# Performance work log

Measured on AMD Instinct MI355X. Metric: run time of the kernel, lower is better.

Reference implementation:

```python
import jax, jax.numpy as jnp
import numpy as np

NUM_EXPERTS = 8
TOP_K = 2
HIDDEN = 1024
INTER = 3584
B, S = 1, 2048


def setup_inputs() -> dict:
    key = jax.random.key(0)
    k0, k1, k2, k3, k4 = jax.random.split(key, 5)
    scale = 0.02
    return {
        "hidden_states": jax.random.normal(k0, (B, S, HIDDEN), dtype=jnp.float32),
        "gate_w": jax.random.normal(k1, (NUM_EXPERTS, HIDDEN), dtype=jnp.float32) * scale,
        "w1": jax.random.normal(k2, (NUM_EXPERTS, INTER, HIDDEN), dtype=jnp.float32) * scale,
        "w2": jax.random.normal(k3, (NUM_EXPERTS, HIDDEN, INTER), dtype=jnp.float32) * scale,
        "w3": jax.random.normal(k4, (NUM_EXPERTS, INTER, HIDDEN), dtype=jnp.float32) * scale,
    }


def reference(hidden_states, gate_w, w1, w2, w3):
    b, s, h = hidden_states.shape
    x = hidden_states.reshape(-1, h)  # [T, H]
    T = x.shape[0]

    # Router: softmax in float32, take top-k, renormalize (normalize_routing_weights=1)
    router_logits = x @ gate_w.T  # [T, E]
    routing_probs = jax.nn.softmax(router_logits.astype(jnp.float32), axis=-1)
    top_w, top_i = jax.lax.top_k(routing_probs, TOP_K)  # [T, K]
    top_w = top_w / jnp.sum(top_w, axis=-1, keepdims=True)
    top_w = top_w.astype(x.dtype)

    # Dense per-token gate matrix [T, E]: weight if expert selected, else 0.
    rows = jnp.arange(T)[:, None]
    gates = jnp.zeros((T, NUM_EXPERTS), dtype=x.dtype).at[rows, top_i].set(top_w)

    # Equivalent to gather-MLP-scatter: y = sum_e gate[:,e] * SwiGLU_e(x)
    out = jnp.zeros((T, h), dtype=x.dtype)
    for e in range(NUM_EXPERTS):
        hid = jax.nn.silu(x @ w1[e].T) * (x @ w3[e].T)  # [T, F]
        out = out + (hid @ w2[e].T) * gates[:, e:e + 1]
    return out.reshape(b, s, h)
```

## Files before the change

kernel.cpp:

```cpp
#include <hip/hip_runtime.h>
#include <hip/hip_bf16.h>
#include <stdint.h>

#define T_TOKENS 2048
#define HID_DIM 1024
#define INTER 3584
#define NEXP 8
#define PTILES 40

typedef float f32x4 __attribute__((ext_vector_type(4)));
typedef short short8 __attribute__((ext_vector_type(8)));
typedef unsigned short ushort8 __attribute__((ext_vector_type(8)));

#define AS1 __attribute__((address_space(1)))
#define AS3 __attribute__((address_space(3)))

__device__ __forceinline__ void gload_lds16(const void* g, void* l) {
    __builtin_amdgcn_global_load_lds((AS1 void*)g, (AS3 void*)l, 16, 0, 0);
}

__device__ __forceinline__ f32x4 mfma16(short8 a, short8 b, f32x4 c) {
    return __builtin_amdgcn_mfma_f32_16x16x32_bf16(a, b, c, 0, 0, 0);
}

__device__ __forceinline__ unsigned short f2bf(float f) {
    union { __hip_bfloat16 h; unsigned short u; } cv;
    cv.h = __float2bfloat16(f);
    return cv.u;
}

__device__ __forceinline__ ushort8 cvt8(float4 v0, float4 v1) {
    ushort8 u;
    u[0] = f2bf(v0.x); u[1] = f2bf(v0.y); u[2] = f2bf(v0.z); u[3] = f2bf(v0.w);
    u[4] = f2bf(v1.x); u[5] = f2bf(v1.y); u[6] = f2bf(v1.z); u[7] = f2bf(v1.w);
    return u;
}

__global__ __launch_bounds__(256) void pack_w_k(const float* __restrict__ w1, const float* __restrict__ w2,
                                                const float* __restrict__ w3,
                                                unsigned short* __restrict__ w1p,
                                                unsigned short* __restrict__ w3p,
                                                unsigned short* __restrict__ w2p) {
    int which = blockIdx.z;
    int e = blockIdx.y;
    const float* src;
    unsigned short* dst;
    int NT, KT, K;
    if (which == 0) { src = w1; dst = w1p; NT = 56; KT = 16; K = HID_DIM; }
    else if (which == 1) { src = w3; dst = w3p; NT = 56; KT = 16; K = HID_DIM; }
    else { src = w2; dst = w2p; NT = 16; KT = 56; K = INTER; }
    int nt = blockIdx.x % NT;
    int kt = blockIdx.x / NT;

    int col = threadIdx.x & 63;
    int kq = threadIdx.x >> 6;
    const float* s = src + ((size_t)(e * (NT * 64) + nt * 64 + col)) * K + kt * 64 + kq * 16;
    float4 v0 = *reinterpret_cast<const float4*>(s);
    float4 v1 = *reinterpret_cast<const float4*>(s + 4);
    float4 v2 = *reinterpret_cast<const float4*>(s + 8);
    float4 v3 = *reinterpret_cast<const float4*>(s + 12);
    unsigned short* d = dst + ((size_t)(e * NT + nt) * KT + kt) * 4096;
    *reinterpret_cast<ushort8*>(d + ((kq * 2 + 0) * 64 + col) * 8) = cvt8(v0, v1);
    *reinterpret_cast<ushort8*>(d + ((kq * 2 + 1) * 64 + col) * 8) = cvt8(v2, v3);
}

__global__ void router_k(const float* __restrict__ x, const float* __restrict__ gw,
                         int* __restrict__ topk_e, float* __restrict__ topk_w,
                         int* __restrict__ ctl) {
    int lane = threadIdx.x & 63;
    int wid = threadIdx.x >> 6;
    int t = blockIdx.x * 4 + wid;
    const float* xr = x + (size_t)t * HID_DIM;

    float acc[NEXP];
#pragma unroll
    for (int e = 0; e < NEXP; ++e) acc[e] = 0.f;

#pragma unroll
    for (int j = 0; j < 4; ++j) {
        int c = j * 256 + lane * 4;
        float4 v = *reinterpret_cast<const float4*>(xr + c);
#pragma unroll
        for (int e = 0; e < NEXP; ++e) {
            float4 g = *reinterpret_cast<const float4*>(gw + e * HID_DIM + c);
            acc[e] += v.x * g.x + v.y * g.y + v.z * g.z + v.w * g.w;
        }
    }
#pragma unroll
    for (int off = 32; off > 0; off >>= 1)
#pragma unroll
        for (int e = 0; e < NEXP; ++e) acc[e] += __shfl_xor(acc[e], off, 64);

    if (lane == 0) {
        int e0 = 0;
#pragma unroll
        for (int e = 1; e < NEXP; ++e) if (acc[e] > acc[e0]) e0 = e;
        int e1 = -1;
        float b1 = 0.f;
#pragma unroll
        for (int e = 0; e < NEXP; ++e) {
            if (e == e0) continue;
            if (e1 < 0 || acc[e] > b1) { e1 = e; b1 = acc[e]; }
        }
        float p1 = __expf(b1 - acc[e0]);
        float s = 1.f + p1;
        topk_e[2 * t] = e0; topk_e[2 * t + 1] = e1;
        topk_w[2 * t] = 1.f / s; topk_w[2 * t + 1] = p1 / s;
        atomicAdd(&ctl[e0], 1);
        atomicAdd(&ctl[e1], 1);
    }
}

__global__ void prefix_k(int* __restrict__ ctl) {
    if (threadIdx.x == 0) {
        int r = 0, ns = 0;
        for (int e = 0; e < NEXP; ++e) {
            ctl[32 + e] = r;
            int c = ctl[e];
            r += (c + 127) & ~127;
            ctl[16 + e] = 0;
            int ntm = (c + 127) >> 7;
            for (int tm = 0; tm < ntm; ++tm) ctl[64 + ns++] = (e << 16) | tm;
        }
        ctl[48] = ns;
    }
}

__global__ void scatter_k(const int* __restrict__ topk_e, const float* __restrict__ topk_w,
                          int* __restrict__ ctl, int* __restrict__ perm_token,
                          float* __restrict__ perm_gate) {
    int t = blockIdx.x * 256 + threadIdx.x;
    if (t >= T_TOKENS) return;
#pragma unroll
    for (int k = 0; k < 2; ++k) {
        int e = topk_e[2 * t + k];
        int p = ctl[32 + e] + atomicAdd(&ctl[16 + e], 1);
        perm_token[p] = t;
        perm_gate[p] = topk_w[2 * t + k];
    }
}

__global__ __launch_bounds__(256) void pack_x_k(const float* __restrict__ x,
                                                const int* __restrict__ perm_token,
                                                unsigned short* __restrict__ xgp) {
    int ptile = blockIdx.x;
    int kt = blockIdx.y;
    int row = threadIdx.x & 127;
    int kh = threadIdx.x >> 7;
    int tok = perm_token[ptile * 128 + row];
    const float* s = x + (size_t)tok * HID_DIM + kt * 64 + kh * 32;
    unsigned short* d = xgp + (size_t)ptile * 131072 + (size_t)kt * 8192;
#pragma unroll
    for (int kb2 = 0; kb2 < 4; ++kb2) {
        int kb = kh * 4 + kb2;
        float4 v0 = *reinterpret_cast<const float4*>(s + kb2 * 8);
        float4 v1 = *reinterpret_cast<const float4*>(s + kb2 * 8 + 4);
        *reinterpret_cast<ushort8*>(d + (kb * 128 + row) * 8) = cvt8(v0, v1);
    }
}

__global__ __launch_bounds__(512, 4) void gemm1_k(
    const unsigned short* __restrict__ xgp,
    const unsigned short* __restrict__ w1p, const unsigned short* __restrict__ w3p,
    const int* __restrict__ ctl, unsigned short* __restrict__ hidp) {
    int ns = ctl[48];
    int slot = blockIdx.x;
    if (slot >= ns) return;
    int et = ctl[64 + slot];
    int e = et >> 16, tm = et & 0xffff;
    int cnt = ctl[e];
    int off = ctl[32 + e];
    int nt = blockIdx.y;
    int ptile = (off >> 7) + tm;

    __shared__ __attribute__((aligned(16))) unsigned short A_l[8192];
    __shared__ __attribute__((aligned(16))) unsigned short B1_l[8192];
    __shared__ __attribute__((aligned(16))) unsigned short B3_l[8192];

    int tid = threadIdx.x;
    int lane = tid & 63;
    int wid = tid >> 6;
    int wr = wid >> 2, wc = wid & 3;
    int q = lane >> 4, rr = lane & 15;

    const unsigned short* asrc = xgp + (size_t)ptile * 131072;
    const unsigned short* b1s0 = w1p + (size_t)(e * 56 + nt * 2) * 65536;
    const unsigned short* b1s1 = b1s0 + 65536;
    const unsigned short* b3s0 = w3p + (size_t)(e * 56 + nt * 2) * 65536;
    const unsigned short* b3s1 = b3s0 + 65536;

    f32x4 acc1[4][2], acc3[4][2];
#pragma unroll
    for (int i = 0; i < 4; ++i)
#pragma unroll
        for (int j = 0; j < 2; ++j) { acc1[i][j] = 0.f; acc3[i][j] = 0.f; }

    int bofs = ((tid >> 6) * 128 + (tid & 63)) * 8;

    for (int kt = 0; kt < 16; ++kt) {
        const unsigned short* as_ = asrc + (size_t)kt * 8192;
        gload_lds16(as_ + tid * 8, A_l + tid * 8);
        gload_lds16(as_ + (512 + tid) * 8, A_l + (512 + tid) * 8);
        gload_lds16(b1s0 + (size_t)kt * 4096 + tid * 8, B1_l + bofs);
        gload_lds16(b1s1 + (size_t)kt * 4096 + tid * 8, B1_l + bofs + 512);
        gload_lds16(b3s0 + (size_t)kt * 4096 + tid * 8, B3_l + bofs);
        gload_lds16(b3s1 + (size_t)kt * 4096 + tid * 8, B3_l + bofs + 512);
        __syncthreads();
#pragma unroll
        for (int kk = 0; kk < 2; ++kk) {
            short8 a[4], b1v[2], b3v[2];
            const unsigned short* abase = A_l + ((kk * 4 + q) * 128 + wr * 64 + rr) * 8;
#pragma unroll
            for (int i = 0; i < 4; ++i) a[i] = *reinterpret_cast<const short8*>(abase + i * 128);
            const unsigned short* b1base = B1_l + ((kk * 4 + q) * 128 + wc * 32 + rr) * 8;
            const unsigned short* b3base = B3_l + ((kk * 4 + q) * 128 + wc * 32 + rr) * 8;
#pragma unroll
            for (int j = 0; j < 2; ++j) {
                b1v[j] = *reinterpret_cast<const short8*>(b1base + j * 128);
                b3v[j] = *reinterpret_cast<const short8*>(b3base + j * 128);
            }
#pragma unroll
            for (int i = 0; i < 4; ++i)
#pragma unroll
                for (int j = 0; j < 2; ++j) {
                    acc1[i][j] = mfma16(a[i], b1v[j], acc1[i][j]);
                    acc3[i][j] = mfma16(a[i], b3v[j], acc3[i][j]);
                }
        }
        __syncthreads();
    }

    int rbase = wr * 64 + q * 4;
#pragma unroll
    for (int i = 0; i < 4; ++i) {
#pragma unroll
        for (int r = 0; r < 4; ++r) {
            int lrow = rbase + i * 16 + r;
            if (tm * 128 + lrow < cnt) {
#pragma unroll
                for (int j = 0; j < 2; ++j) {
                    int cw = wc * 32 + j * 16 + rr;
                    int tile = nt * 2 + (cw >> 6);
                    int cl = cw & 63;
                    float g = acc1[i][j][r];
                    float u = acc3[i][j][r];
                    float h = (g / (1.f + __expf(-g))) * u;
                    hidp[(size_t)(ptile * 56 + tile) * 8192 + ((cl >> 3) * 128 + lrow) * 8 + (cl & 7)] = f2bf(h);
                }
            }
        }
    }
}

__global__ __launch_bounds__(256) void gemm2_k(
    const unsigned short* __restrict__ hidp, const unsigned short* __restrict__ w2p,
    const int* __restrict__ ctl, const int* __restrict__ perm_token,
    const float* __restrict__ perm_gate, float* __restrict__ out) {
    int ns = ctl[48];
    int slot = blockIdx.x;
    if (slot >= ns) return;
    int et = ctl[64 + slot];
    int e = et >> 16, tm = et & 0xffff;
    int ks = blockIdx.z;
    int cnt = ctl[e];
    int off = ctl[32 + e];
    int ptile = (off >> 7) + tm;

    __shared__ __attribute__((aligned(16))) unsigned short A_l[8192];
    __shared__ __attribute__((aligned(16))) unsigned short B_l[8192];

    int tid = threadIdx.x;
    int lane = tid & 63;
    int wid = tid >> 6;
    int wr = wid >> 1, wc = wid & 1;
    int q = lane >> 4, rr = lane & 15;

    const unsigned short* asrc = hidp + (size_t)(ptile * 56) * 8192;
    const unsigned short* bs0 = w2p + (size_t)(e * 16 + 2 * blockIdx.y) * 229376;
    const unsigned short* bs1 = bs0 + 229376;

    f32x4 acc[4][4];
#pragma unroll
    for (int i = 0; i < 4; ++i)
#pragma unroll
        for (int j = 0; j < 4; ++j) acc[i][j] = 0.f;

    int kt0 = ks * 28;
    for (int t = 0; t < 28; ++t) {
        int kt = kt0 + t;
        const unsigned short* as_ = asrc + (size_t)kt * 8192;
        const unsigned short* b0_ = bs0 + (size_t)kt * 4096;
        const unsigned short* b1_ = bs1 + (size_t)kt * 4096;
#pragma unroll
        for (int c = 0; c < 4; ++c)
            gload_lds16(as_ + (c * 256 + tid) * 8, A_l + (c * 256 + tid) * 8);
        gload_lds16(b0_ + tid * 8, B_l + tid * 8);
        gload_lds16(b0_ + (256 + tid) * 8, B_l + (256 + tid) * 8);
        gload_lds16(b1_ + tid * 8, B_l + 4096 + tid * 8);
        gload_lds16(b1_ + (256 + tid) * 8, B_l + 4096 + (256 + tid) * 8);
        __syncthreads();
#pragma unroll
        for (int kk = 0; kk < 2; ++kk) {
            short8 a[4], b[4];
            const unsigned short* abase = A_l + ((kk * 4 + q) * 128 + wr * 64 + rr) * 8;
            const unsigned short* bbase = B_l + wc * 4096 + ((kk * 4 + q) * 64 + rr) * 8;
#pragma unroll
            for (int i = 0; i < 4; ++i) a[i] = *reinterpret_cast<const short8*>(abase + i * 128);
#pragma unroll
            for (int j = 0; j < 4; ++j) b[j] = *reinterpret_cast<const short8*>(bbase + j * 128);
#pragma unroll
            for (int i = 0; i < 4; ++i)
#pragma unroll
                for (int j = 0; j < 4; ++j) acc[i][j] = mfma16(a[i], b[j], acc[i][j]);
        }
        __syncthreads();
    }

    int rb = wr * 64 + q * 4;
    int hb = blockIdx.y * 128 + wc * 64 + rr;
#pragma unroll
    for (int i = 0; i < 4; ++i) {
#pragma unroll
        for (int r = 0; r < 4; ++r) {
            int lrow = rb + i * 16 + r;
            int grow = tm * 128 + lrow;
            if (grow < cnt) {
                int p = off + grow;
                int tok = perm_token[p];
                float gate = perm_gate[p];
#pragma unroll
                for (int j = 0; j < 4; ++j)
                    atomicAdd(&out[(size_t)tok * HID_DIM + hb + j * 16], acc[i][j][r] * gate);
            }
        }
    }
}

extern "C" void kernel_launch(void* const* d_in, const int* in_sizes, int n_in,
                              void* d_out, int out_size, void* d_ws, size_t ws_size,
                              hipStream_t stream) {
    const float* x  = (const float*)d_in[0];
    const float* gw = (const float*)d_in[1];
    const float* w1 = (const float*)d_in[2];
    const float* w2 = (const float*)d_in[3];
    const float* w3 = (const float*)d_in[4];
    float* out = (float*)d_out;

    char* ws = (char*)d_ws;
    int*   ctl        = (int*)ws;
    int*   topk_e     = (int*)(ws + 4096);
    float* topk_w     = (float*)(ws + 20480);
    int*   perm_token = (int*)(ws + 36864);
    float* perm_gate  = (float*)(ws + 57344);
    unsigned short* xgp  = (unsigned short*)(ws + (1ull << 20));
    unsigned short* hidp = (unsigned short*)(ws + 12582912);
    unsigned short* w1p  = (unsigned short*)(ws + 52428800);
    unsigned short* w3p  = (unsigned short*)(ws + 111149056);
    unsigned short* w2p  = (unsigned short*)(ws + 169869312);

    hipMemsetAsync(ctl, 0, 512, stream);
    hipMemsetAsync(perm_token, 0, PTILES * 128 * sizeof(int), stream);
    hipMemsetAsync(out, 0, (size_t)out_size * sizeof(float), stream);

    pack_w_k<<<dim3(896, NEXP, 3), 256, 0, stream>>>(w1, w2, w3, w1p, w3p, w2p);
    router_k<<<dim3(T_TOKENS / 4), 256, 0, stream>>>(x, gw, topk_e, topk_w, ctl);
    prefix_k<<<dim3(1), 64, 0, stream>>>(ctl);
    scatter_k<<<dim3(T_TOKENS / 256), 256, 0, stream>>>(topk_e, topk_w, ctl, perm_token, perm_gate);
    pack_x_k<<<dim3(PTILES, 16), 256, 0, stream>>>(x, perm_token, xgp);
    gemm1_k<<<dim3(PTILES, 28, 1), 512, 0, stream>>>(xgp, w1p, w3p, ctl, hidp);
    gemm2_k<<<dim3(PTILES, HID_DIM / 128, 2), 256, 0, stream>>>(hidp, w2p, ctl, perm_token, perm_gate, out);
}
```

Baseline: 357.7 us.

## Split weight packing into per-matrix kernels and remap GEMM grids for locality

Weight packing is split into two kernels. Each thread now reads contiguous 64-float row segments, so global reads along K are coalesced instead of strided by row across lanes. The GEMM launches also remap block indices: eight consecutive blocks cover different slots that share the same N tile. The aim is that concurrently running blocks reuse the same weight tiles in L2/MALL. The remap assumes exactly 40 slots (8x5) and adds a little index arithmetic.

```diff
diff --git a/kernel.cpp b/kernel.cpp
--- a/kernel.cpp
+++ b/kernel.cpp
@@ -36,32 +36,49 @@
     return u;
 }
 
-__global__ __launch_bounds__(256) void pack_w_k(const float* __restrict__ w1, const float* __restrict__ w2,
-                                                const float* __restrict__ w3,
+__global__ __launch_bounds__(256) void pack13_k(const float* __restrict__ w1, const float* __restrict__ w3,
                                                 unsigned short* __restrict__ w1p,
-                                                unsigned short* __restrict__ w3p,
-                                                unsigned short* __restrict__ w2p) {
-    int which = blockIdx.z;
-    int e = blockIdx.y;
-    const float* src;
-    unsigned short* dst;
-    int NT, KT, K;
-    if (which == 0) { src = w1; dst = w1p; NT = 56; KT = 16; K = HID_DIM; }
-    else if (which == 1) { src = w3; dst = w3p; NT = 56; KT = 16; K = HID_DIM; }
-    else { src = w2; dst = w2p; NT = 16; KT = 56; K = INTER; }
-    int nt = blockIdx.x % NT;
-    int kt = blockIdx.x / NT;
-
-    int col = threadIdx.x & 63;
-    int kq = threadIdx.x >> 6;
-    const float* s = src + ((size_t)(e * (NT * 64) + nt * 64 + col)) * K + kt * 64 + kq * 16;
-    float4 v0 = *reinterpret_cast<const float4*>(s);
-    float4 v1 = *reinterpret_cast<const float4*>(s + 4);
-    float4 v2 = *reinterpret_cast<const float4*>(s + 8);
-    float4 v3 = *reinterpret_cast<const float4*>(s + 12);
-    unsigned short* d = dst + ((size_t)(e * NT + nt) * KT + kt) * 4096;
-    *reinterpret_cast<ushort8*>(d + ((kq * 2 + 0) * 64 + col) * 8) = cvt8(v0, v1);
-    *reinterpret_cast<ushort8*>(d + ((kq * 2 + 1) * 64 + col) * 8) = cvt8(v2, v3);
+                                                unsigned short* __restrict__ w3p) {
+    const float* src = blockIdx.z ? w3 : w1;
+    unsigned short* dst = blockIdx.z ? w3p : w1p;
+    int e = blockIdx.y, nt = blockIdx.x;
+    int kt = threadIdx.x & 15;
+    int r0 = threadIdx.x >> 4;
+    const float* s = src + ((size_t)e * INTER + nt * 64) * HID_DIM + kt * 64;
+    unsigned short* d = dst + (size_t)(e * 56 + nt) * 65536 + kt * 4096;
+#pragma unroll
+    for (int p = 0; p < 4; ++p) {
+        int row = p * 16 + r0;
+        const float* sp = s + (size_t)row * HID_DIM;
+        unsigned short* dp = d + row * 8;
+#pragma unroll
+        for (int kb = 0; kb < 8; ++kb) {
+            float4 v0 = *reinterpret_cast<const float4*>(sp + kb * 8);
+            float4 v1 = *reinterpret_cast<const float4*>(sp + kb * 8 + 4);
+            *reinterpret_cast<ushort8*>(dp + kb * 512) = cvt8(v0, v1);
+        }
+    }
+}
+
+__global__ __launch_bounds__(256) void pack2_k(const float* __restrict__ w2,
+                                               unsigned short* __restrict__ w2p) {
+    int e = blockIdx.y, nt = blockIdx.x, kg = blockIdx.z;
+    int ktl = threadIdx.x & 7;
+    int r0 = threadIdx.x >> 3;
+    const float* s = w2 + ((size_t)e * HID_DIM + nt * 64) * INTER + kg * 512 + ktl * 64;
+    unsigned short* d = w2p + (size_t)(e * 16 + nt) * 229376 + (size_t)(kg * 8 + ktl) * 4096;
+#pragma unroll
+    for (int p = 0; p < 2; ++p) {
+        int row = p * 32 + r0;
+        const float* sp = s + (size_t)row * INTER;
+        unsigned short* dp = d + row * 8;
+#pragma unroll
+        for (int kb = 0; kb < 8; ++kb) {
+            float4 v0 = *reinterpret_cast<const float4*>(sp + kb * 8);
+            float4 v1 = *reinterpret_cast<const float4*>(sp + kb * 8 + 4);
+            *reinterpret_cast<ushort8*>(dp + kb * 512) = cvt8(v0, v1);
+        }
+    }
 }
 
 __global__ void router_k(const float* __restrict__ x, const float* __restrict__ gw,
@@ -164,13 +181,13 @@
     const unsigned short* __restrict__ w1p, const unsigned short* __restrict__ w3p,
     const int* __restrict__ ctl, unsigned short* __restrict__ hidp) {
     int ns = ctl[48];
-    int slot = blockIdx.x;
+    int nt = blockIdx.x >> 3;
+    int slot = (blockIdx.x & 7) * 5 + blockIdx.y;
     if (slot >= ns) return;
     int et = ctl[64 + slot];
     int e = et >> 16, tm = et & 0xffff;
     int cnt = ctl[e];
     int off = ctl[32 + e];
-    int nt = blockIdx.y;
     int ptile = (off >> 7) + tm;
 
     __shared__ __attribute__((aligned(16))) unsigned short A_l[8192];
@@ -257,7 +274,8 @@
     const int* __restrict__ ctl, const int* __restrict__ perm_token,
     const float* __restrict__ perm_gate, float* __restrict__ out) {
     int ns = ctl[48];
-    int slot = blockIdx.x;
+    int nty = blockIdx.x >> 3;
+    int slot = (blockIdx.x & 7) * 5 + blockIdx.y;
     if (slot >= ns) return;
     int et = ctl[64 + slot];
     int e = et >> 16, tm = et & 0xffff;
@@ -276,7 +294,7 @@
     int q = lane >> 4, rr = lane & 15;
 
     const unsigned short* asrc = hidp + (size_t)(ptile * 56) * 8192;
-    const unsigned short* bs0 = w2p + (size_t)(e * 16 + 2 * blockIdx.y) * 229376;
+    const unsigned short* bs0 = w2p + (size_t)(e * 16 + 2 * nty) * 229376;
     const unsigned short* bs1 = bs0 + 229376;
 
     f32x4 acc[4][4];
@@ -317,7 +335,7 @@
     }
 
     int rb = wr * 64 + q * 4;
-    int hb = blockIdx.y * 128 + wc * 64 + rr;
+    int hb = nty * 128 + wc * 64 + rr;
 #pragma unroll
     for (int i = 0; i < 4; ++i) {
 #pragma unroll
@@ -362,11 +380,12 @@
     hipMemsetAsync(perm_token, 0, PTILES * 128 * sizeof(int), stream);
     hipMemsetAsync(out, 0, (size_t)out_size * sizeof(float), stream);
 
-    pack_w_k<<<dim3(896, NEXP, 3), 256, 0, stream>>>(w1, w2, w3, w1p, w3p, w2p);
+    pack13_k<<<dim3(56, NEXP, 2), 256, 0, stream>>>(w1, w3, w1p, w3p);
+    pack2_k<<<dim3(16, NEXP, 7), 256, 0, stream>>>(w2, w2p);
     router_k<<<dim3(T_TOKENS / 4), 256, 0, stream>>>(x, gw, topk_e, topk_w, ctl);
     prefix_k<<<dim3(1), 64, 0, stream>>>(ctl);
     scatter_k<<<dim3(T_TOKENS / 256), 256, 0, stream>>>(topk_e, topk_w, ctl, perm_token, perm_gate);
     pack_x_k<<<dim3(PTILES, 16), 256, 0, stream>>>(x, perm_token, xgp);
-    gemm1_k<<<dim3(PTILES, 28, 1), 512, 0, stream>>>(xgp, w1p, w3p, ctl, hidp);
-    gemm2_k<<<dim3(PTILES, HID_DIM / 128, 2), 256, 0, stream>>>(hidp, w2p, ctl, perm_token, perm_gate, out);
-}
+    gemm1_k<<<dim3(224, 5), 512, 0, stream>>>(xgp, w1p, w3p, ctl, hidp);
+    gemm2_k<<<dim3(64, 5, 2), 256, 0, stream>>>(hidp, w2p, ctl, perm_token, perm_gate, out);
+}
```

Measured after the change: 379.7 us. +6.2%, slower.

## Fuse weight fp32-to-bf16 conversion into GEMM loads and drop weight pack kernel

Applied to the files above, without the earlier changes.

Removes the separate pack_w_k pass, which converted all three expert weight tensors to bf16 tiles on every call. The GEMMs now read fp32 weights directly into registers, convert them to bf16 and store them into LDS, prefetching the next K-tile during compute. The grid is also remapped so blocks sharing a weight tile run close together, and gemm2 moves to 512 threads with 256-wide N tiles. In exchange the fp32 weights are read at double width inside the GEMM, conversion ALU work is added there, and the async LDS loads for B are replaced by register staging.

```diff
diff --git a/kernel.cpp b/kernel.cpp
--- a/kernel.cpp
+++ b/kernel.cpp
@@ -34,34 +34,6 @@
     u[0] = f2bf(v0.x); u[1] = f2bf(v0.y); u[2] = f2bf(v0.z); u[3] = f2bf(v0.w);
     u[4] = f2bf(v1.x); u[5] = f2bf(v1.y); u[6] = f2bf(v1.z); u[7] = f2bf(v1.w);
     return u;
-}
-
-__global__ __launch_bounds__(256) void pack_w_k(const float* __restrict__ w1, const float* __restrict__ w2,
-                                                const float* __restrict__ w3,
-                                                unsigned short* __restrict__ w1p,
-                                                unsigned short* __restrict__ w3p,
-                                                unsigned short* __restrict__ w2p) {
-    int which = blockIdx.z;
-    int e = blockIdx.y;
-    const float* src;
-    unsigned short* dst;
-    int NT, KT, K;
-    if (which == 0) { src = w1; dst = w1p; NT = 56; KT = 16; K = HID_DIM; }
-    else if (which == 1) { src = w3; dst = w3p; NT = 56; KT = 16; K = HID_DIM; }
-    else { src = w2; dst = w2p; NT = 16; KT = 56; K = INTER; }
-    int nt = blockIdx.x % NT;
-    int kt = blockIdx.x / NT;
-
-    int col = threadIdx.x & 63;
-    int kq = threadIdx.x >> 6;
-    const float* s = src + ((size_t)(e * (NT * 64) + nt * 64 + col)) * K + kt * 64 + kq * 16;
-    float4 v0 = *reinterpret_cast<const float4*>(s);
-    float4 v1 = *reinterpret_cast<const float4*>(s + 4);
-    float4 v2 = *reinterpret_cast<const float4*>(s + 8);
-    float4 v3 = *reinterpret_cast<const float4*>(s + 12);
-    unsigned short* d = dst + ((size_t)(e * NT + nt) * KT + kt) * 4096;
-    *reinterpret_cast<ushort8*>(d + ((kq * 2 + 0) * 64 + col) * 8) = cvt8(v0, v1);
-    *reinterpret_cast<ushort8*>(d + ((kq * 2 + 1) * 64 + col) * 8) = cvt8(v2, v3);
 }
 
 __global__ void router_k(const float* __restrict__ x, const float* __restrict__ gw,
@@ -159,18 +131,18 @@
     }
 }
 
-__global__ __launch_bounds__(512, 4) void gemm1_k(
+__global__ __launch_bounds__(512) void gemm1_k(
     const unsigned short* __restrict__ xgp,
-    const unsigned short* __restrict__ w1p, const unsigned short* __restrict__ w3p,
+    const float* __restrict__ w1, const float* __restrict__ w3,
     const int* __restrict__ ctl, unsigned short* __restrict__ hidp) {
     int ns = ctl[48];
-    int slot = blockIdx.x;
+    int nt = blockIdx.x >> 3;
+    int slot = (blockIdx.x & 7) * 5 + blockIdx.y;
     if (slot >= ns) return;
     int et = ctl[64 + slot];
     int e = et >> 16, tm = et & 0xffff;
     int cnt = ctl[e];
     int off = ctl[32 + e];
-    int nt = blockIdx.y;
     int ptile = (off >> 7) + tm;
 
     __shared__ __attribute__((aligned(16))) unsigned short A_l[8192];
@@ -184,10 +156,13 @@
     int q = lane >> 4, rr = lane & 15;
 
     const unsigned short* asrc = xgp + (size_t)ptile * 131072;
-    const unsigned short* b1s0 = w1p + (size_t)(e * 56 + nt * 2) * 65536;
-    const unsigned short* b1s1 = b1s0 + 65536;
-    const unsigned short* b3s0 = w3p + (size_t)(e * 56 + nt * 2) * 65536;
-    const unsigned short* b3s1 = b3s0 + 65536;
+
+    int col = tid & 127;
+    int kh = tid >> 7;
+    const float* b1s = w1 + ((size_t)e * INTER + nt * 128 + col) * HID_DIM + kh * 16;
+    const float* b3s = w3 + ((size_t)e * INTER + nt * 128 + col) * HID_DIM + kh * 16;
+    int bo0 = ((kh * 2 + 0) * 128 + col) * 8;
+    int bo1 = ((kh * 2 + 1) * 128 + col) * 8;
 
     f32x4 acc1[4][2], acc3[4][2];
 #pragma unroll
@@ -195,17 +170,31 @@
 #pragma unroll
         for (int j = 0; j < 2; ++j) { acc1[i][j] = 0.f; acc3[i][j] = 0.f; }
 
-    int bofs = ((tid >> 6) * 128 + (tid & 63)) * 8;
-
+    float4 r10, r11, r12, r13, r30, r31, r32, r33;
+#define G1_LOADB(KT) do {                                                     \
+        const float* p1_ = b1s + (size_t)(KT) * 64;                           \
+        const float* p3_ = b3s + (size_t)(KT) * 64;                           \
+        r10 = *reinterpret_cast<const float4*>(p1_);                          \
+        r11 = *reinterpret_cast<const float4*>(p1_ + 4);                      \
+        r12 = *reinterpret_cast<const float4*>(p1_ + 8);                      \
+        r13 = *reinterpret_cast<const float4*>(p1_ + 12);                     \
+        r30 = *reinterpret_cast<const float4*>(p3_);                          \
+        r31 = *reinterpret_cast<const float4*>(p3_ + 4);                      \
+        r32 = *reinterpret_cast<const float4*>(p3_ + 8);                      \
+        r33 = *reinterpret_cast<const float4*>(p3_ + 12);                     \
+    } while (0)
+
+    G1_LOADB(0);
     for (int kt = 0; kt < 16; ++kt) {
         const unsigned short* as_ = asrc + (size_t)kt * 8192;
         gload_lds16(as_ + tid * 8, A_l + tid * 8);
         gload_lds16(as_ + (512 + tid) * 8, A_l + (512 + tid) * 8);
-        gload_lds16(b1s0 + (size_t)kt * 4096 + tid * 8, B1_l + bofs);
-        gload_lds16(b1s1 + (size_t)kt * 4096 + tid * 8, B1_l + bofs + 512);
-        gload_lds16(b3s0 + (size_t)kt * 4096 + tid * 8, B3_l + bofs);
-        gload_lds16(b3s1 + (size_t)kt * 4096 + tid * 8, B3_l + bofs + 512);
+        *reinterpret_cast<ushort8*>(B1_l + bo0) = cvt8(r10, r11);
+        *reinterpret_cast<ushort8*>(B1_l + bo1) = cvt8(r12, r13);
+        *reinterpret_cast<ushort8*>(B3_l + bo0) = cvt8(r30, r31);
+        *reinterpret_cast<ushort8*>(B3_l + bo1) = cvt8(r32, r33);
         __syncthreads();
+        if (kt < 15) G1_LOADB(kt + 1);
 #pragma unroll
         for (int kk = 0; kk < 2; ++kk) {
             short8 a[4], b1v[2], b3v[2];
@@ -229,6 +218,7 @@
         }
         __syncthreads();
     }
+#undef G1_LOADB
 
     int rbase = wr * 64 + q * 4;
 #pragma unroll
@@ -252,12 +242,13 @@
     }
 }
 
-__global__ __launch_bounds__(256) void gemm2_k(
-    const unsigned short* __restrict__ hidp, const unsigned short* __restrict__ w2p,
+__global__ __launch_bounds__(512) void gemm2_k(
+    const unsigned short* __restrict__ hidp, const float* __restrict__ w2,
     const int* __restrict__ ctl, const int* __restrict__ perm_token,
     const float* __restrict__ perm_gate, float* __restrict__ out) {
     int ns = ctl[48];
-    int slot = blockIdx.x;
+    int nt = blockIdx.x >> 3;
+    int slot = (blockIdx.x & 7) * 5 + blockIdx.y;
     if (slot >= ns) return;
     int et = ctl[64 + slot];
     int e = et >> 16, tm = et & 0xffff;
@@ -267,17 +258,23 @@
     int ptile = (off >> 7) + tm;
 
     __shared__ __attribute__((aligned(16))) unsigned short A_l[8192];
-    __shared__ __attribute__((aligned(16))) unsigned short B_l[8192];
+    __shared__ __attribute__((aligned(16))) unsigned short B_l[16384];
 
     int tid = threadIdx.x;
     int lane = tid & 63;
     int wid = tid >> 6;
-    int wr = wid >> 1, wc = wid & 1;
+    int wr = wid >> 2, wc = wid & 3;
     int q = lane >> 4, rr = lane & 15;
 
     const unsigned short* asrc = hidp + (size_t)(ptile * 56) * 8192;
-    const unsigned short* bs0 = w2p + (size_t)(e * 16 + 2 * blockIdx.y) * 229376;
-    const unsigned short* bs1 = bs0 + 229376;
+
+    int col = tid & 255;
+    int kh = tid >> 8;
+    const float* bs = w2 + ((size_t)e * HID_DIM + nt * 256 + col) * INTER + kh * 32;
+    int bo0 = ((kh * 4 + 0) * 256 + col) * 8;
+    int bo1 = ((kh * 4 + 1) * 256 + col) * 8;
+    int bo2 = ((kh * 4 + 2) * 256 + col) * 8;
+    int bo3 = ((kh * 4 + 3) * 256 + col) * 8;
 
     f32x4 acc[4][4];
 #pragma unroll
@@ -285,25 +282,37 @@
 #pragma unroll
         for (int j = 0; j < 4; ++j) acc[i][j] = 0.f;
 
+    float4 s0, s1, s2, s3, s4, s5, s6, s7;
+#define G2_LOADB(KT) do {                                                     \
+        const float* p_ = bs + (size_t)(KT) * 64;                             \
+        s0 = *reinterpret_cast<const float4*>(p_);                            \
+        s1 = *reinterpret_cast<const float4*>(p_ + 4);                        \
+        s2 = *reinterpret_cast<const float4*>(p_ + 8);                        \
+        s3 = *reinterpret_cast<const float4*>(p_ + 12);                       \
+        s4 = *reinterpret_cast<const float4*>(p_ + 16);                       \
+        s5 = *reinterpret_cast<const float4*>(p_ + 20);                       \
+        s6 = *reinterpret_cast<const float4*>(p_ + 24);                       \
+        s7 = *reinterpret_cast<const float4*>(p_ + 28);                       \
+    } while (0)
+
     int kt0 = ks * 28;
+    G2_LOADB(kt0);
     for (int t = 0; t < 28; ++t) {
         int kt = kt0 + t;
         const unsigned short* as_ = asrc + (size_t)kt * 8192;
-        const unsigned short* b0_ = bs0 + (size_t)kt * 4096;
-        const unsigned short* b1_ = bs1 + (size_t)kt * 4096;
-#pragma unroll
-        for (int c = 0; c < 4; ++c)
-            gload_lds16(as_ + (c * 256 + tid) * 8, A_l + (c * 256 + tid) * 8);
-        gload_lds16(b0_ + tid * 8, B_l + tid * 8);
-        gload_lds16(b0_ + (256 + tid) * 8, B_l + (256 + tid) * 8);
-        gload_lds16(b1_ + tid * 8, B_l + 4096 + tid * 8);
-        gload_lds16(b1_ + (256 + tid) * 8, B_l + 4096 + (256 + tid) * 8);
+        gload_lds16(as_ + tid * 8, A_l + tid * 8);
+        gload_lds16(as_ + (512 + tid) * 8, A_l + (512 + tid) * 8);
+        *reinterpret_cast<ushort8*>(B_l + bo0) = cvt8(s0, s1);
+        *reinterpret_cast<ushort8*>(B_l + bo1) = cvt8(s2, s3);
+        *reinterpret_cast<ushort8*>(B_l + bo2) = cvt8(s4, s5);
+        *reinterpret_cast<ushort8*>(B_l + bo3) = cvt8(s6, s7);
         __syncthreads();
+        if (t < 27) G2_LOADB(kt + 1);
 #pragma unroll
         for (int kk = 0; kk < 2; ++kk) {
             short8 a[4], b[4];
             const unsigned short* abase = A_l + ((kk * 4 + q) * 128 + wr * 64 + rr) * 8;
-            const unsigned short* bbase = B_l + wc * 4096 + ((kk * 4 + q) * 64 + rr) * 8;
+            const unsigned short* bbase = B_l + ((kk * 4 + q) * 256 + wc * 64 + rr) * 8;
 #pragma unroll
             for (int i = 0; i < 4; ++i) a[i] = *reinterpret_cast<const short8*>(abase + i * 128);
 #pragma unroll
@@ -315,9 +324,10 @@
         }
         __syncthreads();
     }
+#undef G2_LOADB
 
     int rb = wr * 64 + q * 4;
-    int hb = blockIdx.y * 128 + wc * 64 + rr;
+    int hb = nt * 256 + wc * 64 + rr;
 #pragma unroll
     for (int i = 0; i < 4; ++i) {
 #pragma unroll
@@ -354,19 +364,15 @@
     float* perm_gate  = (float*)(ws + 57344);
     unsigned short* xgp  = (unsigned short*)(ws + (1ull << 20));
     unsigned short* hidp = (unsigned short*)(ws + 12582912);
-    unsigned short* w1p  = (unsigned short*)(ws + 52428800);
-    unsigned short* w3p  = (unsigned short*)(ws + 111149056);
-    unsigned short* w2p  = (unsigned short*)(ws + 169869312);
 
     hipMemsetAsync(ctl, 0, 512, stream);
     hipMemsetAsync(perm_token, 0, PTILES * 128 * sizeof(int), stream);
     hipMemsetAsync(out, 0, (size_t)out_size * sizeof(float), stream);
 
-    pack_w_k<<<dim3(896, NEXP, 3), 256, 0, stream>>>(w1, w2, w3, w1p, w3p, w2p);
     router_k<<<dim3(T_TOKENS / 4), 256, 0, stream>>>(x, gw, topk_e, topk_w, ctl);
     prefix_k<<<dim3(1), 64, 0, stream>>>(ctl);
     scatter_k<<<dim3(T_TOKENS / 256), 256, 0, stream>>>(topk_e, topk_w, ctl, perm_token, perm_gate);
     pack_x_k<<<dim3(PTILES, 16), 256, 0, stream>>>(x, perm_token, xgp);
-    gemm1_k<<<dim3(PTILES, 28, 1), 512, 0, stream>>>(xgp, w1p, w3p, ctl, hidp);
-    gemm2_k<<<dim3(PTILES, HID_DIM / 128, 2), 256, 0, stream>>>(hidp, w2p, ctl, perm_token, perm_gate, out);
-}
+    gemm1_k<<<dim3(224, 5), 512, 0, stream>>>(xgp, w1, w3, ctl, hidp);
+    gemm2_k<<<dim3(32, 5, 2), 512, 0, stream>>>(hidp, w2, ctl, perm_token, perm_gate, out);
+}
```

New measurement: 596.8 us. 66.9% more time.

## Replace tiled weight packing with plain bf16 conversion and swizzled LDS loads

Applied to the files above, without the earlier changes.

The weight pre-pack kernel no longer rearranges w1/w2/w3 into tile-major blocks. It now does a flat element-wise fp32-to-bf16 conversion that streams contiguously. The GEMM kernels load weight rows directly from the row-major bf16 copies and use an XOR swizzle in LDS so the fragment reads avoid bank conflicts. The grid is also remapped so that consecutive blocks share the same weight N-tile across different token slots, which should improve L2 reuse of weights. The trade-off is strided row reads of 16B chunks in the GEMM instead of fully contiguous tile loads.

```diff
diff --git a/kernel.cpp b/kernel.cpp
--- a/kernel.cpp
+++ b/kernel.cpp
@@ -36,32 +36,23 @@
     return u;
 }
 
-__global__ __launch_bounds__(256) void pack_w_k(const float* __restrict__ w1, const float* __restrict__ w2,
-                                                const float* __restrict__ w3,
-                                                unsigned short* __restrict__ w1p,
-                                                unsigned short* __restrict__ w3p,
-                                                unsigned short* __restrict__ w2p) {
-    int which = blockIdx.z;
-    int e = blockIdx.y;
+__global__ __launch_bounds__(256) void cvt_k(const float* __restrict__ w1, const float* __restrict__ w2,
+                                             const float* __restrict__ w3,
+                                             unsigned short* __restrict__ w1b,
+                                             unsigned short* __restrict__ w2b,
+                                             unsigned short* __restrict__ w3b) {
     const float* src;
     unsigned short* dst;
-    int NT, KT, K;
-    if (which == 0) { src = w1; dst = w1p; NT = 56; KT = 16; K = HID_DIM; }
-    else if (which == 1) { src = w3; dst = w3p; NT = 56; KT = 16; K = HID_DIM; }
-    else { src = w2; dst = w2p; NT = 16; KT = 56; K = INTER; }
-    int nt = blockIdx.x % NT;
-    int kt = blockIdx.x / NT;
-
-    int col = threadIdx.x & 63;
-    int kq = threadIdx.x >> 6;
-    const float* s = src + ((size_t)(e * (NT * 64) + nt * 64 + col)) * K + kt * 64 + kq * 16;
-    float4 v0 = *reinterpret_cast<const float4*>(s);
-    float4 v1 = *reinterpret_cast<const float4*>(s + 4);
-    float4 v2 = *reinterpret_cast<const float4*>(s + 8);
-    float4 v3 = *reinterpret_cast<const float4*>(s + 12);
-    unsigned short* d = dst + ((size_t)(e * NT + nt) * KT + kt) * 4096;
-    *reinterpret_cast<ushort8*>(d + ((kq * 2 + 0) * 64 + col) * 8) = cvt8(v0, v1);
-    *reinterpret_cast<ushort8*>(d + ((kq * 2 + 1) * 64 + col) * 8) = cvt8(v2, v3);
+    if (blockIdx.z == 0) { src = w1; dst = w1b; }
+    else if (blockIdx.z == 1) { src = w3; dst = w3b; }
+    else { src = w2; dst = w2b; }
+    size_t i = ((size_t)blockIdx.x * 256 + threadIdx.x) * 16;
+    float4 v0 = *reinterpret_cast<const float4*>(src + i);
+    float4 v1 = *reinterpret_cast<const float4*>(src + i + 4);
+    float4 v2 = *reinterpret_cast<const float4*>(src + i + 8);
+    float4 v3 = *reinterpret_cast<const float4*>(src + i + 12);
+    *reinterpret_cast<ushort8*>(dst + i) = cvt8(v0, v1);
+    *reinterpret_cast<ushort8*>(dst + i + 8) = cvt8(v2, v3);
 }
 
 __global__ void router_k(const float* __restrict__ x, const float* __restrict__ gw,
@@ -161,16 +152,16 @@
 
 __global__ __launch_bounds__(512, 4) void gemm1_k(
     const unsigned short* __restrict__ xgp,
-    const unsigned short* __restrict__ w1p, const unsigned short* __restrict__ w3p,
+    const unsigned short* __restrict__ w1b, const unsigned short* __restrict__ w3b,
     const int* __restrict__ ctl, unsigned short* __restrict__ hidp) {
     int ns = ctl[48];
-    int slot = blockIdx.x;
+    int nt = blockIdx.x >> 3;
+    int slot = (blockIdx.x & 7) * 5 + blockIdx.y;
     if (slot >= ns) return;
     int et = ctl[64 + slot];
     int e = et >> 16, tm = et & 0xffff;
     int cnt = ctl[e];
     int off = ctl[32 + e];
-    int nt = blockIdx.y;
     int ptile = (off >> 7) + tm;
 
     __shared__ __attribute__((aligned(16))) unsigned short A_l[8192];
@@ -184,27 +175,28 @@
     int q = lane >> 4, rr = lane & 15;
 
     const unsigned short* asrc = xgp + (size_t)ptile * 131072;
-    const unsigned short* b1s0 = w1p + (size_t)(e * 56 + nt * 2) * 65536;
-    const unsigned short* b1s1 = b1s0 + 65536;
-    const unsigned short* b3s0 = w3p + (size_t)(e * 56 + nt * 2) * 65536;
-    const unsigned short* b3s1 = b3s0 + 65536;
+
+    int col0 = tid >> 3;
+    int c0 = tid & 7;
+    int swzc = c0 ^ (col0 & 7);
+    size_t rowbase = (size_t)(e * INTER + nt * 128) * HID_DIM;
+    const unsigned short* b1r = w1b + rowbase + (size_t)col0 * HID_DIM + swzc * 8;
+    const unsigned short* b3r = w3b + rowbase + (size_t)col0 * HID_DIM + swzc * 8;
 
     f32x4 acc1[4][2], acc3[4][2];
 #pragma unroll
     for (int i = 0; i < 4; ++i)
 #pragma unroll
         for (int j = 0; j < 2; ++j) { acc1[i][j] = 0.f; acc3[i][j] = 0.f; }
-
-    int bofs = ((tid >> 6) * 128 + (tid & 63)) * 8;
 
     for (int kt = 0; kt < 16; ++kt) {
         const unsigned short* as_ = asrc + (size_t)kt * 8192;
         gload_lds16(as_ + tid * 8, A_l + tid * 8);
         gload_lds16(as_ + (512 + tid) * 8, A_l + (512 + tid) * 8);
-        gload_lds16(b1s0 + (size_t)kt * 4096 + tid * 8, B1_l + bofs);
-        gload_lds16(b1s1 + (size_t)kt * 4096 + tid * 8, B1_l + bofs + 512);
-        gload_lds16(b3s0 + (size_t)kt * 4096 + tid * 8, B3_l + bofs);
-        gload_lds16(b3s1 + (size_t)kt * 4096 + tid * 8, B3_l + bofs + 512);
+        gload_lds16(b1r + kt * 64, B1_l + tid * 8);
+        gload_lds16(b1r + (size_t)64 * HID_DIM + kt * 64, B1_l + (512 + tid) * 8);
+        gload_lds16(b3r + kt * 64, B3_l + tid * 8);
+        gload_lds16(b3r + (size_t)64 * HID_DIM + kt * 64, B3_l + (512 + tid) * 8);
         __syncthreads();
 #pragma unroll
         for (int kk = 0; kk < 2; ++kk) {
@@ -212,12 +204,13 @@
             const unsigned short* abase = A_l + ((kk * 4 + q) * 128 + wr * 64 + rr) * 8;
 #pragma unroll
             for (int i = 0; i < 4; ++i) a[i] = *reinterpret_cast<const short8*>(abase + i * 128);
-            const unsigned short* b1base = B1_l + ((kk * 4 + q) * 128 + wc * 32 + rr) * 8;
-            const unsigned short* b3base = B3_l + ((kk * 4 + q) * 128 + wc * 32 + rr) * 8;
+            int swz = ((kk * 4 + q) ^ (rr & 7)) * 8;
+            const unsigned short* b1base = B1_l + (wc * 32 + rr) * 64 + swz;
+            const unsigned short* b3base = B3_l + (wc * 32 + rr) * 64 + swz;
 #pragma unroll
             for (int j = 0; j < 2; ++j) {
-                b1v[j] = *reinterpret_cast<const short8*>(b1base + j * 128);
-                b3v[j] = *reinterpret_cast<const short8*>(b3base + j * 128);
+                b1v[j] = *reinterpret_cast<const short8*>(b1base + j * 1024);
+                b3v[j] = *reinterpret_cast<const short8*>(b3base + j * 1024);
             }
 #pragma unroll
             for (int i = 0; i < 4; ++i)
@@ -253,11 +246,12 @@
 }
 
 __global__ __launch_bounds__(256) void gemm2_k(
-    const unsigned short* __restrict__ hidp, const unsigned short* __restrict__ w2p,
+    const unsigned short* __restrict__ hidp, const unsigned short* __restrict__ w2b,
     const int* __restrict__ ctl, const int* __restrict__ perm_token,
     const float* __restrict__ perm_gate, float* __restrict__ out) {
     int ns = ctl[48];
-    int slot = blockIdx.x;
+    int nty = blockIdx.x >> 3;
+    int slot = (blockIdx.x & 7) * 5 + blockIdx.y;
     if (slot >= ns) return;
     int et = ctl[64 + slot];
     int e = et >> 16, tm = et & 0xffff;
@@ -276,8 +270,11 @@
     int q = lane >> 4, rr = lane & 15;
 
     const unsigned short* asrc = hidp + (size_t)(ptile * 56) * 8192;
-    const unsigned short* bs0 = w2p + (size_t)(e * 16 + 2 * blockIdx.y) * 229376;
-    const unsigned short* bs1 = bs0 + 229376;
+
+    int colg0 = tid >> 3;
+    int c0 = tid & 7;
+    int swzc = c0 ^ (colg0 & 7);
+    const unsigned short* b2r = w2b + (size_t)(e * HID_DIM + nty * 128 + colg0) * INTER + swzc * 8;
 
     f32x4 acc[4][4];
 #pragma unroll
@@ -289,25 +286,23 @@
     for (int t = 0; t < 28; ++t) {
         int kt = kt0 + t;
         const unsigned short* as_ = asrc + (size_t)kt * 8192;
-        const unsigned short* b0_ = bs0 + (size_t)kt * 4096;
-        const unsigned short* b1_ = bs1 + (size_t)kt * 4096;
 #pragma unroll
         for (int c = 0; c < 4; ++c)
             gload_lds16(as_ + (c * 256 + tid) * 8, A_l + (c * 256 + tid) * 8);
-        gload_lds16(b0_ + tid * 8, B_l + tid * 8);
-        gload_lds16(b0_ + (256 + tid) * 8, B_l + (256 + tid) * 8);
-        gload_lds16(b1_ + tid * 8, B_l + 4096 + tid * 8);
-        gload_lds16(b1_ + (256 + tid) * 8, B_l + 4096 + (256 + tid) * 8);
+#pragma unroll
+        for (int i = 0; i < 4; ++i)
+            gload_lds16(b2r + (size_t)i * 32 * INTER + kt * 64, B_l + (i * 256 + tid) * 8);
         __syncthreads();
 #pragma unroll
         for (int kk = 0; kk < 2; ++kk) {
             short8 a[4], b[4];
             const unsigned short* abase = A_l + ((kk * 4 + q) * 128 + wr * 64 + rr) * 8;
-            const unsigned short* bbase = B_l + wc * 4096 + ((kk * 4 + q) * 64 + rr) * 8;
+            int swz = ((kk * 4 + q) ^ (rr & 7)) * 8;
+            const unsigned short* bbase = B_l + wc * 4096 + rr * 64 + swz;
 #pragma unroll
             for (int i = 0; i < 4; ++i) a[i] = *reinterpret_cast<const short8*>(abase + i * 128);
 #pragma unroll
-            for (int j = 0; j < 4; ++j) b[j] = *reinterpret_cast<const short8*>(bbase + j * 128);
+            for (int j = 0; j < 4; ++j) b[j] = *reinterpret_cast<const short8*>(bbase + j * 1024);
 #pragma unroll
             for (int i = 0; i < 4; ++i)
 #pragma unroll
@@ -317,7 +312,7 @@
     }
 
     int rb = wr * 64 + q * 4;
-    int hb = blockIdx.y * 128 + wc * 64 + rr;
+    int hb = nty * 128 + wc * 64 + rr;
 #pragma unroll
     for (int i = 0; i < 4; ++i) {
 #pragma unroll
@@ -354,19 +349,19 @@
     float* perm_gate  = (float*)(ws + 57344);
     unsigned short* xgp  = (unsigned short*)(ws + (1ull << 20));
     unsigned short* hidp = (unsigned short*)(ws + 12582912);
-    unsigned short* w1p  = (unsigned short*)(ws + 52428800);
-    unsigned short* w3p  = (unsigned short*)(ws + 111149056);
-    unsigned short* w2p  = (unsigned short*)(ws + 169869312);
+    unsigned short* w1b  = (unsigned short*)(ws + 52428800);
+    unsigned short* w3b  = (unsigned short*)(ws + 111149056);
+    unsigned short* w2b  = (unsigned short*)(ws + 169869312);
 
     hipMemsetAsync(ctl, 0, 512, stream);
     hipMemsetAsync(perm_token, 0, PTILES * 128 * sizeof(int), stream);
     hipMemsetAsync(out, 0, (size_t)out_size * sizeof(float), stream);
 
-    pack_w_k<<<dim3(896, NEXP, 3), 256, 0, stream>>>(w1, w2, w3, w1p, w3p, w2p);
+    cvt_k<<<dim3(7168, 1, 3), 256, 0, stream>>>(w1, w2, w3, w1b, w2b, w3b);
     router_k<<<dim3(T_TOKENS / 4), 256, 0, stream>>>(x, gw, topk_e, topk_w, ctl);
     prefix_k<<<dim3(1), 64, 0, stream>>>(ctl);
     scatter_k<<<dim3(T_TOKENS / 256), 256, 0, stream>>>(topk_e, topk_w, ctl, perm_token, perm_gate);
     pack_x_k<<<dim3(PTILES, 16), 256, 0, stream>>>(x, perm_token, xgp);
-    gemm1_k<<<dim3(PTILES, 28, 1), 512, 0, stream>>>(xgp, w1p, w3p, ctl, hidp);
-    gemm2_k<<<dim3(PTILES, HID_DIM / 128, 2), 256, 0, stream>>>(hidp, w2p, ctl, perm_token, perm_gate, out);
-}
+    gemm1_k<<<dim3(224, 5), 512, 0, stream>>>(xgp, w1b, w3b, ctl, hidp);
+    gemm2_k<<<dim3(64, 5, 2), 256, 0, stream>>>(hidp, w2b, ctl, perm_token, perm_gate, out);
+}
```

After: 341.0 us. -4.7%, faster.
